# Performance work log

Hardware: AMD Instinct MI355X
Metric: run time of the kernel (lower is better)

## Reference

```python
import jax, jax.numpy as jnp
import numpy as np

N_EMBD = 2048
N_HEAD = 16
N_INNER = 8192
EPS = 1e-5


def _wn_weight(v, g):
    # torch weight_norm with dim=1 on weight [out, in]:
    # w[:, j] = g[j] * v[:, j] / ||v[:, j]||_2
    norm = jnp.sqrt(jnp.sum(v * v, axis=0))  # [in]
    return v * (g / norm)[None, :]


def _layer_norm(x, gamma, beta):
    mu = jnp.mean(x, axis=-1, keepdims=True)
    var = jnp.mean(jnp.square(x - mu), axis=-1, keepdims=True)
    return (x - mu) * jax.lax.rsqrt(var + EPS) * gamma + beta


def setup_inputs() -> dict:
    key = jax.random.key(0)
    ks = jax.random.split(key, 12)
    E, I, H = N_EMBD, N_INNER, N_HEAD
    s = lambda n: 1.0 / np.sqrt(n)
    return {
        "hidden_states": jax.random.normal(ks[0], (2, 2048, E), jnp.float32),
        "ln1_g": jnp.ones((E,), jnp.float32),
        "ln1_b": jnp.zeros((E,), jnp.float32),
        "w_qkv": jax.random.normal(ks[1], (3 * E, E), jnp.float32) * s(E),
        "b_qkv": jnp.zeros((3 * E,), jnp.float32),
        "attn_proj_v": jax.random.normal(ks[2], (E, E), jnp.float32) * s(E),
        "attn_proj_g": jnp.abs(jax.random.normal(ks[3], (E,), jnp.float32)) + 0.5,
        "attn_proj_b": jnp.zeros((E,), jnp.float32),
        "emotion_bias": jax.random.normal(ks[4], (H,), jnp.float32) * 0.1,
        "ln2_g": jnp.ones((E,), jnp.float32),
        "ln2_b": jnp.zeros((E,), jnp.float32),
        "w_fc": jax.random.normal(ks[5], (I, E), jnp.float32) * s(E),
        "b_fc": jnp.zeros((I,), jnp.float32),
        "mlp_proj_v": jax.random.normal(ks[6], (E, I), jnp.float32) * s(I),
        "mlp_proj_g": jnp.abs(jax.random.normal(ks[7], (I,), jnp.float32)) + 0.5,
        "mlp_proj_b": jnp.zeros((E,), jnp.float32),
    }


def reference(hidden_states, ln1_g, ln1_b, w_qkv, b_qkv, attn_proj_v, attn_proj_g,
              attn_proj_b, emotion_bias, ln2_g, ln2_b, w_fc, b_fc,
              mlp_proj_v, mlp_proj_g, mlp_proj_b):
    B, S, E = hidden_states.shape
    H = N_HEAD
    D = E // H

    # --- attention sub-block ---
    residual = hidden_states
    x = _layer_norm(hidden_states, ln1_g, ln1_b)
    qkv = x @ w_qkv.T + b_qkv                       # [B,S,3E]
    q, k, v = jnp.split(qkv, 3, axis=-1)
    q = q.reshape(B, S, H, D).transpose(0, 2, 1, 3)  # [B,H,S,D]
    k = k.reshape(B, S, H, D).transpose(0, 2, 1, 3)
    v = v.reshape(B, S, H, D).transpose(0, 2, 1, 3)

    scores = jnp.einsum("bhqd,bhkd->bhqk", q, k) / jnp.sqrt(jnp.float32(D))
    scores = scores + emotion_bias[None, :, None, None]
    probs = jax.nn.softmax(scores, axis=-1)
    attn = jnp.einsum("bhqk,bhkd->bhqd", probs, v)   # [B,H,S,D]
    attn = attn.transpose(0, 2, 1, 3).reshape(B, S, E)
    w_proj = _wn_weight(attn_proj_v, attn_proj_g)
    attn = attn @ w_proj.T + attn_proj_b

    hidden = attn + residual

    # --- MLP sub-block ---
    residual = hidden
    x = _layer_norm(hidden, ln2_g, ln2_b)
    h = jax.nn.gelu(x @ w_fc.T + b_fc, approximate=False)
    w_proj2 = _wn_weight(mlp_proj_v, mlp_proj_g)
    h = h @ w_proj2.T + mlp_proj_b
    return residual + h
```

## Files before the change

kernel.cpp:

```cpp
#include <hip/hip_runtime.h>
#include <hip/hip_bf16.h>

#define DEVI __device__ __forceinline__

typedef __attribute__((ext_vector_type(8))) __bf16 bf16x8;
typedef __attribute__((ext_vector_type(4))) float f32x4;
typedef __attribute__((ext_vector_type(4))) unsigned short u16x4;
typedef __attribute__((ext_vector_type(8))) unsigned short u16x8;

DEVI unsigned short f2bf(float f) {
  unsigned int u = __float_as_uint(f);
  u += 0x7FFFu + ((u >> 16) & 1u);
  return (unsigned short)(u >> 16);
}
DEVI float bf2f(unsigned short u) {
  return __uint_as_float(((unsigned int)u) << 16);
}

#define GLD16(g, l) __builtin_amdgcn_global_load_lds(                      \
    (const __attribute__((address_space(1))) void*)(g),                    \
    (__attribute__((address_space(3))) void*)(l), 16, 0, 0)


__global__ __launch_bounds__(256) void cast_k(const float* __restrict__ in,
                                              unsigned short* __restrict__ out,
                                              int n4) {
  for (int i = blockIdx.x * 256 + threadIdx.x; i < n4; i += gridDim.x * 256) {
    f32x4 v = ((const f32x4*)in)[i];
    u16x4 o;
    o.x = f2bf(v.x); o.y = f2bf(v.y); o.z = f2bf(v.z); o.w = f2bf(v.w);
    ((u16x4*)out)[i] = o;
  }
}

__global__ __launch_bounds__(256) void colnorm1_k(const float* __restrict__ v,
                                                  float* __restrict__ part,
                                                  int cols) {
  const int tid = threadIdx.x;
  const int g = tid & 127;
  const int s = tid >> 7;
  const int c0 = blockIdx.x * 512;
  const int r0 = blockIdx.y * 64 + s * 32;
  const float* base = v + (size_t)r0 * cols + c0 + g * 4;
  f32x4 acc = {};
#pragma unroll 4
  for (int i = 0; i < 32; ++i) {
    f32x4 x = *(const f32x4*)(base + (size_t)i * cols);
    acc.x += x.x * x.x; acc.y += x.y * x.y;
    acc.z += x.z * x.z; acc.w += x.w * x.w;
  }
  __shared__ f32x4 red[256];
  red[tid] = acc;
  __syncthreads();
  if (s == 0) {
    f32x4 a = red[tid], b = red[tid + 128];
    f32x4 o;
    o.x = a.x + b.x; o.y = a.y + b.y; o.z = a.z + b.z; o.w = a.w + b.w;
    *(f32x4*)(part + (size_t)blockIdx.y * cols + c0 + g * 4) = o;
  }
}

__global__ __launch_bounds__(256) void colnorm2_k(const float* __restrict__ part,
                                                  const float* __restrict__ g,
                                                  float* __restrict__ s,
                                                  int cols, int nrc) {
  const int c = blockIdx.x * 256 + threadIdx.x;
  float acc = 0.f;
  for (int i = 0; i < nrc; ++i) acc += part[(size_t)i * cols + c];
  s[c] = g[c] * rsqrtf(acc);
}

__global__ __launch_bounds__(256) void scale_cast_k(const float* __restrict__ in,
                                                    const float* __restrict__ s,
                                                    unsigned short* __restrict__ out,
                                                    int cols, int n4) {
  const int cmask4 = (cols >> 2) - 1;
  for (int i = blockIdx.x * 256 + threadIdx.x; i < n4; i += gridDim.x * 256) {
    f32x4 v = ((const f32x4*)in)[i];
    f32x4 sv = ((const f32x4*)s)[i & cmask4];
    u16x4 o;
    o.x = f2bf(v.x * sv.x); o.y = f2bf(v.y * sv.y);
    o.z = f2bf(v.z * sv.z); o.w = f2bf(v.w * sv.w);
    ((u16x4*)out)[i] = o;
  }
}

__global__ __launch_bounds__(256) void ln_k(const float* __restrict__ x,
                                            const float* __restrict__ g,
                                            const float* __restrict__ b,
                                            unsigned short* __restrict__ out) {
  const int tid = threadIdx.x, lane = tid & 63, wid = tid >> 6;
  const int row = blockIdx.x;
  const float* xr = x + (size_t)row * 2048;
  f32x4 a0 = ((const f32x4*)xr)[tid];
  f32x4 a1 = ((const f32x4*)xr)[tid + 256];
  float s = a0.x + a0.y + a0.z + a0.w + a1.x + a1.y + a1.z + a1.w;
  float ss = a0.x * a0.x + a0.y * a0.y + a0.z * a0.z + a0.w * a0.w +
             a1.x * a1.x + a1.y * a1.y + a1.z * a1.z + a1.w * a1.w;
#pragma unroll
  for (int m = 1; m < 64; m <<= 1) {
    s += __shfl_xor(s, m);
    ss += __shfl_xor(ss, m);
  }
  __shared__ float red[8];
  if (lane == 0) { red[wid] = s; red[4 + wid] = ss; }
  __syncthreads();
  s = red[0] + red[1] + red[2] + red[3];
  ss = red[4] + red[5] + red[6] + red[7];
  const float mu = s * (1.f / 2048.f);
  const float var = ss * (1.f / 2048.f) - mu * mu;
  const float rs = rsqrtf(var + 1e-5f);
  f32x4 g0 = ((const f32x4*)g)[tid], g1 = ((const f32x4*)g)[tid + 256];
  f32x4 b0 = ((const f32x4*)b)[tid], b1 = ((const f32x4*)b)[tid + 256];
  u16x4 o0, o1;
  o0.x = f2bf((a0.x - mu) * rs * g0.x + b0.x);
  o0.y = f2bf((a0.y - mu) * rs * g0.y + b0.y);
  o0.z = f2bf((a0.z - mu) * rs * g0.z + b0.z);
  o0.w = f2bf((a0.w - mu) * rs * g0.w + b0.w);
  o1.x = f2bf((a1.x - mu) * rs * g1.x + b1.x);
  o1.y = f2bf((a1.y - mu) * rs * g1.y + b1.y);
  o1.z = f2bf((a1.z - mu) * rs * g1.z + b1.z);
  o1.w = f2bf((a1.w - mu) * rs * g1.w + b1.w);
  unsigned short* orow = out + (size_t)row * 2048;
  *(u16x4*)(orow + 4 * tid) = o0;
  *(u16x4*)(orow + 1024 + 4 * tid) = o1;
}

__global__ __launch_bounds__(256) void vtrans_k(const unsigned short* __restrict__ qkv,
                                                unsigned short* __restrict__ vt) {
  __shared__ unsigned short t[64][134];
  const int tid = threadIdx.x;
  const int bh = blockIdx.x >> 5, st = blockIdx.x & 31;
  const int b = bh >> 4, h = bh & 15;
  const unsigned short* vb = qkv + (size_t)(b * 2048 + st * 64) * 6144 + 4096 + h * 128;
#pragma unroll
  for (int i = 0; i < 4; ++i) {
    int f = tid + (i << 8);
    int row = f >> 4, c8 = f & 15;
    u16x8 x = *(const u16x8*)(vb + (size_t)row * 6144 + c8 * 8);
#pragma unroll
    for (int j = 0; j < 4; ++j) {
      unsigned int pk = ((unsigned int)x[2 * j + 1] << 16) | x[2 * j];
      *(unsigned int*)&t[row][c8 * 8 + 2 * j] = pk;
    }
  }
  __syncthreads();
  const int lane = tid & 63, wid = tid >> 6;
  unsigned short* ob = vt + ((size_t)bh << 18) + (st << 6);
#pragma unroll
  for (int j = 0; j < 32; ++j) {
    int d = (wid << 5) + j;
    ob[((size_t)d << 11) + lane] = t[lane][d];
  }
}

__global__ __launch_bounds__(256) void g4red_k(const unsigned short* __restrict__ parts,
                                               const float* __restrict__ bias,
                                               const float* __restrict__ res,
                                               float* __restrict__ out, int n4) {
  const size_t PS = (size_t)4096 * 2048;
  for (int i = blockIdx.x * 256 + threadIdx.x; i < n4; i += gridDim.x * 256) {
    u16x4 a = ((const u16x4*)(parts))[i];
    u16x4 b = ((const u16x4*)(parts + PS))[i];
    u16x4 c = ((const u16x4*)(parts + 2 * PS))[i];
    u16x4 d = ((const u16x4*)(parts + 3 * PS))[i];
    f32x4 r = ((const f32x4*)res)[i];
    f32x4 bb = ((const f32x4*)bias)[i & 511];
    f32x4 o;
    o.x = bf2f(a.x) + bf2f(b.x) + bf2f(c.x) + bf2f(d.x) + r.x + bb.x;
    o.y = bf2f(a.y) + bf2f(b.y) + bf2f(c.y) + bf2f(d.y) + r.y + bb.y;
    o.z = bf2f(a.z) + bf2f(b.z) + bf2f(c.z) + bf2f(d.z) + r.z + bb.z;
    o.w = bf2f(a.w) + bf2f(b.w) + bf2f(c.w) + bf2f(d.w) + r.w + bb.w;
    ((f32x4*)out)[i] = o;
  }
}

struct GemmP {
  const unsigned short* A;
  const unsigned short* B;
  const float* bias;
  const float* res;
  float* outF;
  unsigned short* outH;
  int M, N, K;
};

DEVI void gemm128_body(const GemmP& p, int m0, int n0, int k0, int nk) {
  const int tid = threadIdx.x, lane = tid & 63, wid = tid >> 6;
  const int K = p.K;
  const int wr = wid >> 1, wc = wid & 1;

  __shared__ __align__(16) unsigned short sA[2][4096];
  __shared__ __align__(16) unsigned short sB[2][4096];

  const int c0 = tid, c1 = tid + 256;
  const unsigned short* gA0 = p.A + (size_t)(m0 + (c0 >> 2)) * K + k0 + ((c0 & 3) << 3);
  const unsigned short* gA1 = p.A + (size_t)(m0 + (c1 >> 2)) * K + k0 + ((c1 & 3) << 3);
  const unsigned short* gB0 = p.B + (size_t)(n0 + (c0 >> 2)) * K + k0 + ((c0 & 3) << 3);
  const unsigned short* gB1 = p.B + (size_t)(n0 + (c1 >> 2)) * K + k0 + ((c1 & 3) << 3);
  const int l0 = wid << 9, l1 = (wid << 9) + 2048;

  f32x4 acc[4][4] = {};
  const int arow = (wr << 6) + (lane & 15);
  const int brow = (wc << 6) + (lane & 15);
  const int koff = (lane >> 4) << 3;

#define STAGE128(bufi, t) do { int ko = (t) << 5;       \
    GLD16(gA0 + ko, &sA[bufi][l0]);                     \
    GLD16(gA1 + ko, &sA[bufi][l1]);                     \
    GLD16(gB0 + ko, &sB[bufi][l0]);                     \
    GLD16(gB1 + ko, &sB[bufi][l1]); } while (0)

  STAGE128(0, 0);
  __syncthreads();
  int cur = 0;
  for (int t = 0; t < nk; ++t) {
    if (t + 1 < nk) STAGE128(cur ^ 1, t + 1);
    bf16x8 af[4], bfr[4];
#pragma unroll
    for (int i = 0; i < 4; ++i)
      af[i] = *(const bf16x8*)&sA[cur][(arow + (i << 4)) * 32 + koff];
#pragma unroll
    for (int i = 0; i < 4; ++i)
      bfr[i] = *(const bf16x8*)&sB[cur][(brow + (i << 4)) * 32 + koff];
#pragma unroll
    for (int i = 0; i < 4; ++i)
#pragma unroll
      for (int j = 0; j < 4; ++j)
        acc[i][j] = __builtin_amdgcn_mfma_f32_16x16x32_bf16(af[i], bfr[j], acc[i][j], 0, 0, 0);
    __syncthreads();
    cur ^= 1;
  }
#undef STAGE128

  const int rbase = m0 + (wr << 6) + ((lane >> 4) << 2);
  const int cbase = n0 + (wc << 6) + (lane & 15);
#pragma unroll
  for (int mi = 0; mi < 4; ++mi) {
#pragma unroll
    for (int ni = 0; ni < 4; ++ni) {
      const int col = cbase + (ni << 4);
#pragma unroll
      for (int r = 0; r < 4; ++r) {
        const int row = rbase + (mi << 4) + r;
        const size_t o = (size_t)row * p.N + col;
        p.outF[o] = acc[mi][ni][r] + p.bias[col] + p.res[o];
      }
    }
  }
}

__global__ __launch_bounds__(256) void g2_proj128(GemmP p) {
  const int x = blockIdx.x & 7, i = blockIdx.x >> 3;
  const int bm = (x >> 1) * 8 + (i >> 3);
  const int bn = (x & 1) * 8 + (i & 7);
  gemm128_body(p, bm << 7, bn << 7, 0, p.K >> 5);
}

DEVI void setup256(const GemmP& p, int m0, int n0, int k0,
                   const unsigned short*& gsA0, const unsigned short*& gsA1,
                   const unsigned short*& gsB0, const unsigned short*& gsB1) {
  const int tid = threadIdx.x;
  int r_[2], c_[2];
#pragma unroll
  for (int j = 0; j < 2; ++j) {
    int d = tid * 16 + j * 8192;
    int w = (d & 1023) ^ (((d >> 9) & 1) << 5);
    r_[j] = ((d >> 10) << 4) + (w >> 6);
    c_[j] = (w & 63) >> 1;
  }
  gsA0 = p.A + (size_t)(m0 + r_[0]) * p.K + k0 + c_[0];
  gsA1 = p.A + (size_t)(m0 + r_[1]) * p.K + k0 + c_[1];
  gsB0 = p.B + (size_t)(n0 + r_[0]) * p.K + k0 + c_[0];
  gsB1 = p.B + (size_t)(n0 + r_[1]) * p.K + k0 + c_[1];
}

template <int EPI>
DEVI void epi256(const GemmP& p, f32x4 (&acc)[8][4], int m0, int n0,
                 unsigned short* outH) {
  const int lane = threadIdx.x & 63, wid = threadIdx.x >> 6;
  const int wr = wid >> 2, wc = wid & 3;
  const int lr = lane & 15, lk = lane >> 4;
  const int rbase = m0 + wr * 128 + (lk << 2);
  const int cbase = n0 + wc * 64 + lr;
#pragma unroll
  for (int m = 0; m < 8; ++m) {
#pragma unroll
    for (int n = 0; n < 4; ++n) {
      const int col = cbase + (n << 4);
      const float bb = (EPI == 5) ? 0.f : p.bias[col];
#pragma unroll
      for (int r = 0; r < 4; ++r) {
        const int row = rbase + (m << 4) + r;
        float v = acc[m][n][r] + bb;
        if constexpr (EPI == 2) {
          float y = 0.7978845608028654f * (v + 0.044715f * v * v * v);
          float u = __expf(2.f * y);
          v = (y > 40.f) ? v : v * (u / (u + 1.f));
        }
        outH[(size_t)row * p.N + col] = f2bf(v);
      }
    }
  }
}

template <int EPI>
DEVI void gemm2p_body(const GemmP& p, unsigned short* lds_raw, int m0, int n0,
                      int k0, int nk, unsigned short* outH) {
  const int tid = threadIdx.x, lane = tid & 63, wid = tid >> 6;
  const int wr = wid >> 2, wc = wid & 3;
  const int lr = lane & 15, lk = lane >> 4;
  const int fb = (lr * 64 + lk * 16) ^ ((lr & 8) << 2);

  const unsigned short *gsA0, *gsA1, *gsB0, *gsB1;
  setup256(p, m0, n0, k0, gsA0, gsA1, gsB0, gsB1);

#define STG2(b, kt) do { unsigned short* _d = lds_raw + ((b) << 14);     \
    GLD16(gsA0 + ((size_t)(kt) << 5), _d + (tid << 3));                  \
    GLD16(gsA1 + ((size_t)(kt) << 5), _d + 4096 + (tid << 3));           \
    GLD16(gsB0 + ((size_t)(kt) << 5), _d + 8192 + (tid << 3));           \
    GLD16(gsB1 + ((size_t)(kt) << 5), _d + 12288 + (tid << 3)); } while (0)

  f32x4 acc[8][4] = {};
  STG2(0, 0);
  __syncthreads();
  int cur = 0;
  for (int t = 0; t < nk; ++t) {
    if (t + 1 < nk) STG2(cur ^ 1, t + 1);
    const char* tA = (const char*)(lds_raw + (cur << 14));
    const char* tB = tA + 16384;
    bf16x8 a_[8], b_[4];
#pragma unroll
    for (int n = 0; n < 4; ++n)
      b_[n] = *(const bf16x8*)(tB + (((wc << 2) + n) << 10) + fb);
#pragma unroll
    for (int m = 0; m < 8; ++m)
      a_[m] = *(const bf16x8*)(tA + (((wr << 3) + m) << 10) + fb);
#pragma unroll
    for (int m = 0; m < 8; ++m)
#pragma unroll
      for (int n = 0; n < 4; ++n)
        acc[m][n] = __builtin_amdgcn_mfma_f32_16x16x32_bf16(a_[m], b_[n], acc[m][n], 0, 0, 0);
    __syncthreads();
    cur ^= 1;
  }
#undef STG2
  epi256<EPI>(p, acc, m0, n0, outH);
}

template <int EPI>
DEVI void gemmr2k64_body(const GemmP& p, unsigned short* lds_raw, int m0, int n0,
                         int k0, int nk64, unsigned short* outH) {
  const int tid = threadIdx.x, lane = tid & 63, wid = tid >> 6;
  const int wr = wid >> 2, wc = wid & 3;
  const int lr = lane & 15, lk = lane >> 4;
  const int fb = (lr * 64 + lk * 16) ^ ((lr & 8) << 2);

  const unsigned short *gsA0, *gsA1, *gsB0, *gsB1;
  setup256(p, m0, n0, k0, gsA0, gsA1, gsB0, gsB1);

#define STG64(bufi, kt) do { unsigned short* _d = lds_raw + ((bufi) << 15);  \
    int _ko = (kt) << 6;                                                     \
    GLD16(gsA0 + _ko,      _d + (tid << 3));                                 \
    GLD16(gsA1 + _ko,      _d + 4096 + (tid << 3));                          \
    GLD16(gsA0 + _ko + 32, _d + 8192 + (tid << 3));                          \
    GLD16(gsA1 + _ko + 32, _d + 12288 + (tid << 3));                         \
    GLD16(gsB0 + _ko,      _d + 16384 + (tid << 3));                         \
    GLD16(gsB1 + _ko,      _d + 20480 + (tid << 3));                         \
    GLD16(gsB0 + _ko + 32, _d + 24576 + (tid << 3));                         \
    GLD16(gsB1 + _ko + 32, _d + 28672 + (tid << 3)); } while (0)

  f32x4 acc[8][4] = {};
  STG64(0, 0);
  asm volatile("s_waitcnt vmcnt(0)" ::: "memory");
  __builtin_amdgcn_s_barrier();
  asm volatile("" ::: "memory");

  for (int t = 0; t < nk64; ++t) {
    if (t + 1 < nk64) STG64((t + 1) & 1, t + 1);
    const char* base = (const char*)(lds_raw + ((t & 1) << 15));
#pragma unroll
    for (int s = 0; s < 2; ++s) {
      const char* tA = base + s * 16384;
      const char* tB = base + 32768 + s * 16384;
      bf16x8 a_[8], b_[4];
#pragma unroll
      for (int n = 0; n < 4; ++n)
        b_[n] = *(const bf16x8*)(tB + (((wc << 2) + n) << 10) + fb);
#pragma unroll
      for (int m = 0; m < 8; ++m)
        a_[m] = *(const bf16x8*)(tA + (((wr << 3) + m) << 10) + fb);
      __builtin_amdgcn_s_setprio(1);
#pragma unroll
      for (int m = 0; m < 8; ++m)
#pragma unroll
        for (int n = 0; n < 4; ++n)
          acc[m][n] = __builtin_amdgcn_mfma_f32_16x16x32_bf16(a_[m], b_[n], acc[m][n], 0, 0, 0);
      __builtin_amdgcn_s_setprio(0);
    }
    if (t + 1 < nk64) asm volatile("s_waitcnt vmcnt(0)" ::: "memory");
    __builtin_amdgcn_s_barrier();
    asm volatile("" ::: "memory");
  }
#undef STG64
  epi256<EPI>(p, acc, m0, n0, outH);
}

__global__ __launch_bounds__(512, 2) void g1_qkv256(GemmP p) {
  extern __shared__ unsigned short lds_raw[];
  const int x = blockIdx.x & 7, i = blockIdx.x >> 3;
  const int bm = (x & 1) * 8 + (i & 7);
  const int bn = (x >> 1) * 6 + (i >> 3);
  gemm2p_body<0>(p, lds_raw, bm << 8, bn << 8, 0, p.K >> 5, p.outH);
}
__global__ __launch_bounds__(512, 1) void g3_fc64(GemmP p) {
  extern __shared__ unsigned short lds_raw[];
  const int x = blockIdx.x & 7, i = blockIdx.x >> 3;
  const int bm = (x & 1) * 8 + (i & 7);
  const int bn = (x >> 1) * 8 + (i >> 3);
  gemmr2k64_body<2>(p, lds_raw, bm << 8, bn << 8, 0, 32, p.outH);
}
__global__ __launch_bounds__(512, 1) void g4_sk64(GemmP p) {
  extern __shared__ unsigned short lds_raw[];
  const int x = blockIdx.x & 7, i = blockIdx.x >> 3;
  const int ks = x & 3;
  const int bm = (x >> 2) * 8 + (i >> 3);
  const int bn = i & 7;
  unsigned short* outH = p.outH + (size_t)ks * 4096 * 2048;
  gemmr2k64_body<5>(p, lds_raw, bm << 8, bn << 8, ks << 11, 32, outH);
}

__global__ __launch_bounds__(512) void attn_k(const unsigned short* __restrict__ qkv,
                                              const unsigned short* __restrict__ Vt,
                                              unsigned short* __restrict__ O) {
  const int tid = threadIdx.x, lane = tid & 63, wid = tid >> 6;
  const int bid = blockIdx.x;
  const int pos = bid >> 3;
  const int bh = (bid & 7) * 4 + (pos >> 4);
  const int qt = pos & 15;
  const int q0 = qt * 128 + wid * 16;
  const int b = bh >> 4, h = bh & 15;
  const float C = 0.08838834764831845f * 1.4426950408889634f;

  __shared__ __align__(16) unsigned short sK[64 * 128];
  __shared__ __align__(16) unsigned short sV[128 * 64];
  __shared__ __align__(16) unsigned short sP[8][16 * 72];

  const unsigned short* Qb = qkv + (size_t)(b * 2048) * 6144 + h * 128;
  const unsigned short* Kb = qkv + (size_t)(b * 2048) * 6144 + 2048 + h * 128;
  const unsigned short* Vb = Vt + ((size_t)bh << 18);

  bf16x8 qf[4];
  {
    const unsigned short* qp = Qb + (size_t)(q0 + (lane & 15)) * 6144 + ((lane >> 4) << 3);
#pragma unroll
    for (int kk = 0; kk < 4; ++kk) qf[kk] = *(const bf16x8*)(qp + kk * 32);
  }

  int koffs[2], voffs[2];
#pragma unroll
  for (int i = 0; i < 2; ++i) {
    const int c = tid + (i << 9);
    const int kv = c >> 4, jj = c & 15;
    const int js = (jj & 8) | ((jj ^ kv) & 7);
    koffs[i] = kv * 6144 + (js << 3);
    const int d = c >> 3, j2 = c & 7;
    const int js2 = j2 ^ (d & 7);
    voffs[i] = d * 2048 + (js2 << 3);
  }
  u16x8 kreg[2], vreg[2];
  auto PREF = [&](int kt) {
    const int kv0 = kt << 6;
    const unsigned short* kb = Kb + (size_t)kv0 * 6144;
#pragma unroll
    for (int i = 0; i < 2; ++i) {
      kreg[i] = *(const u16x8*)(kb + koffs[i]);
      vreg[i] = *(const u16x8*)(Vb + kv0 + voffs[i]);
    }
  };

  f32x4 oacc[8] = {};
  float mrun = -3e38f, lrun = 0.f;
  PREF(0);

  for (int kt = 0; kt < 32; ++kt) {
#pragma unroll
    for (int i = 0; i < 2; ++i) {
      const int c8 = (tid + (i << 9)) << 3;
      *(u16x8*)&sK[c8] = kreg[i];
      *(u16x8*)&sV[c8] = vreg[i];
    }
    __syncthreads();
    if (kt + 1 < 32) PREF(kt + 1);

    f32x4 sc[4] = {};
    __builtin_amdgcn_s_setprio(1);
#pragma unroll
    for (int ti = 0; ti < 4; ++ti) {
#pragma unroll
      for (int kk = 0; kk < 4; ++kk) {
        const int row = (ti << 4) + (lane & 15);
        int bo = (row << 8) + (kk << 6) + ((lane >> 4) << 4);
        bo ^= (row & 7) << 4;
        bf16x8 kf = *(const bf16x8*)((const char*)sK + bo);
        sc[ti] = __builtin_amdgcn_mfma_f32_16x16x32_bf16(kf, qf[kk], sc[ti], 0, 0, 0);
      }
    }
    __builtin_amdgcn_s_setprio(0);

    float pv[16];
    float mx = -3e38f;
#pragma unroll
    for (int ti = 0; ti < 4; ++ti)
#pragma unroll
      for (int r = 0; r < 4; ++r) {
        float x = sc[ti][r];
        pv[(ti << 2) + r] = x;
        mx = fmaxf(mx, x);
      }
    mx = fmaxf(mx, __shfl_xor(mx, 16));
    mx = fmaxf(mx, __shfl_xor(mx, 32));

    float corr = 1.f;
    if (!__all(mx - mrun <= 90.50966799f)) {
      const float mnew = fmaxf(mrun, mx);
      corr = exp2f((mrun - mnew) * C);
      mrun = mnew;
      float fr[4];
#pragma unroll
      for (int r = 0; r < 4; ++r) fr[r] = __shfl(corr, ((lane >> 4) << 2) + r);
#pragma unroll
      for (int di = 0; di < 8; ++di)
#pragma unroll
        for (int r = 0; r < 4; ++r) oacc[di][r] *= fr[r];
    }
    float psum = 0.f;
#pragma unroll
    for (int i2 = 0; i2 < 16; ++i2) {
      float e = exp2f((pv[i2] - mrun) * C);
      pv[i2] = e;
      psum += e;
    }
    psum += __shfl_xor(psum, 16);
    psum += __shfl_xor(psum, 32);
    lrun = lrun * corr + psum;

    unsigned short* prow = &sP[wid][(lane & 15) * 72];
#pragma unroll
    for (int ti = 0; ti < 4; ++ti) {
      u16x4 w4;
      w4.x = f2bf(pv[(ti << 2) + 0]);
      w4.y = f2bf(pv[(ti << 2) + 1]);
      w4.z = f2bf(pv[(ti << 2) + 2]);
      w4.w = f2bf(pv[(ti << 2) + 3]);
      *(u16x4*)&prow[(ti << 4) + ((lane >> 4) << 2)] = w4;
    }

    bf16x8 pfA, pfB;
    {
      const char* pb = (const char*)&sP[wid][0] + (lane & 15) * 144 + ((lane >> 4) << 4);
      pfA = *(const bf16x8*)(pb);
      pfB = *(const bf16x8*)(pb + 64);
    }
    __builtin_amdgcn_s_setprio(1);
#pragma unroll
    for (int di = 0; di < 8; ++di) {
#pragma unroll
      for (int ks = 0; ks < 2; ++ks) {
        const int dr = (di << 4) + (lane & 15);
        int bo = (dr << 7) + (ks << 6) + ((lane >> 4) << 4);
        bo ^= (dr & 7) << 4;
        bf16x8 vf = *(const bf16x8*)((const char*)sV + bo);
        oacc[di] = __builtin_amdgcn_mfma_f32_16x16x32_bf16(ks ? pfB : pfA, vf, oacc[di], 0, 0, 0);
      }
    }
    __builtin_amdgcn_s_setprio(0);
    __syncthreads();
  }

  float il[4];
#pragma unroll
  for (int r = 0; r < 4; ++r) il[r] = 1.f / __shfl(lrun, ((lane >> 4) << 2) + r);
  const size_t obase = ((size_t)(b * 2048 + q0)) * 2048 + h * 128;
#pragma unroll
  for (int di = 0; di < 8; ++di)
#pragma unroll
    for (int r = 0; r < 4; ++r) {
      const size_t o = obase + (size_t)(((lane >> 4) << 2) + r) * 2048 + (di << 4) + (lane & 15);
      O[o] = f2bf(oacc[di][r] * il[r]);
    }
}


extern "C" void kernel_launch(void* const* d_in, const int* in_sizes, int n_in,
                              void* d_out, int out_size, void* d_ws, size_t ws_size,
                              hipStream_t stream) {
  (void)in_sizes; (void)n_in; (void)out_size; (void)ws_size;
  const float* hidden = (const float*)d_in[0];
  const float* ln1_g = (const float*)d_in[1];
  const float* ln1_b = (const float*)d_in[2];
  const float* w_qkv = (const float*)d_in[3];
  const float* b_qkv = (const float*)d_in[4];
  const float* apv = (const float*)d_in[5];
  const float* apg = (const float*)d_in[6];
  const float* apb = (const float*)d_in[7];
  const float* ln2_g = (const float*)d_in[9];
  const float* ln2_b = (const float*)d_in[10];
  const float* w_fc = (const float*)d_in[11];
  const float* b_fc = (const float*)d_in[12];
  const float* mpv = (const float*)d_in[13];
  const float* mpg = (const float*)d_in[14];
  const float* mpb = (const float*)d_in[15];

  char* w = (char*)d_ws;
  const size_t MBs = 1ull << 20;
  unsigned short* xln = (unsigned short*)(w + 0);
  float* hidden2 = (float*)(w + 0);
  unsigned short* vtbuf = (unsigned short*)(w + 32 * MBs);
  unsigned short* hbuf = (unsigned short*)(w + 32 * MBs);
  unsigned short* qkv = (unsigned short*)(w + 96 * MBs);
  unsigned short* wfc_bf = (unsigned short*)(w + 96 * MBs);
  unsigned short* partH = (unsigned short*)(w + 96 * MBs);
  unsigned short* xln2 = (unsigned short*)(w + 128 * MBs);
  unsigned short* attn_out = (unsigned short*)(w + 144 * MBs);
  unsigned short* wqkv_bf = (unsigned short*)(w + 160 * MBs);
  unsigned short* w2_bf = (unsigned short*)(w + 160 * MBs);
  unsigned short* wproj_bf = (unsigned short*)(w + 192 * MBs);
  float* s_attn = (float*)(w + 200 * MBs);
  float* s_mlp = (float*)(w + 200 * MBs + 32768);
  float* part_attn = (float*)(w + 201 * MBs);
  float* part_mlp = (float*)(w + 202 * MBs);

  hipFuncSetAttribute((const void*)g1_qkv256, hipFuncAttributeMaxDynamicSharedMemorySize, 65536);
  hipFuncSetAttribute((const void*)g3_fc64, hipFuncAttributeMaxDynamicSharedMemorySize, 131072);
  hipFuncSetAttribute((const void*)g4_sk64, hipFuncAttributeMaxDynamicSharedMemorySize, 131072);

  cast_k<<<2048, 256, 0, stream>>>(w_qkv, wqkv_bf, (6144 * 2048) / 4);
  colnorm1_k<<<dim3(4, 32), 256, 0, stream>>>(apv, part_attn, 2048);
  colnorm2_k<<<8, 256, 0, stream>>>(part_attn, apg, s_attn, 2048, 32);
  scale_cast_k<<<2048, 256, 0, stream>>>(apv, s_attn, wproj_bf, 2048, (2048 * 2048) / 4);
  colnorm1_k<<<dim3(16, 32), 256, 0, stream>>>(mpv, part_mlp, 8192);
  colnorm2_k<<<32, 256, 0, stream>>>(part_mlp, mpg, s_mlp, 8192, 32);

  ln_k<<<4096, 256, 0, stream>>>(hidden, ln1_g, ln1_b, xln);

  GemmP p1 = {xln, wqkv_bf, b_qkv, nullptr, nullptr, qkv, 4096, 6144, 2048};
  g1_qkv256<<<384, 512, 65536, stream>>>(p1);

  vtrans_k<<<1024, 256, 0, stream>>>(qkv, vtbuf);

  attn_k<<<512, 512, 0, stream>>>(qkv, vtbuf, attn_out);

  cast_k<<<2048, 256, 0, stream>>>(w_fc, wfc_bf, (8192 * 2048) / 4);
  scale_cast_k<<<4096, 256, 0, stream>>>(mpv, s_mlp, w2_bf, 8192, (2048 * 8192) / 4);

  GemmP p2 = {attn_out, wproj_bf, apb, hidden, hidden2, nullptr, 4096, 2048, 2048};
  g2_proj128<<<512, 256, 0, stream>>>(p2);

  ln_k<<<4096, 256, 0, stream>>>(hidden2, ln2_g, ln2_b, xln2);

  GemmP p3 = {xln2, wfc_bf, b_fc, nullptr, nullptr, hbuf, 4096, 8192, 2048};
  g3_fc64<<<512, 512, 131072, stream>>>(p3);

  GemmP p4 = {hbuf, w2_bf, mpb, nullptr, nullptr, partH, 4096, 2048, 8192};
  g4_sk64<<<512, 512, 131072, stream>>>(p4);
  g4red_k<<<2048, 256, 0, stream>>>(partH, mpb, hidden2, (float*)d_out,
                                    (4096 * 2048) / 4);
}
```

Baseline: 735.8 us.

## Use 8-phase ping-pong pipelined GEMM body for FC layer

```diff
diff --git a/kernel.cpp b/kernel.cpp
--- a/kernel.cpp
+++ b/kernel.cpp
@@ -406,6 +406,99 @@
   epi256<EPI>(p, acc, m0, n0, outH);
 }
 
+template <int EPI>
+DEVI void gemm8p_body(const GemmP& p, unsigned short* lds_raw, int m0, int n0,
+                      int k0, int nt, unsigned short* outH) {
+  const int tid = threadIdx.x, lane = tid & 63, wid = tid >> 6;
+  const int wr = wid >> 2, wc = wid & 3;
+  const int lr = lane & 15, lk = lane >> 4;
+  const int fb = (lr * 64 + lk * 16) ^ ((lr & 8) << 2);
+  char* Lc = (char*)lds_raw;
+
+  const unsigned short *gsA0, *gsA1, *gsB0, *gsB1;
+  setup256(p, m0, n0, k0, gsA0, gsA1, gsB0, gsB1);
+
+#define STGH(bufb, h, gp, tt) do {                                        \
+    char* _d = Lc + ((bufb) << 16) + ((h) << 14) + tid * 16;              \
+    GLD16((gp) + ((size_t)(tt) << 6),      _d);                           \
+    GLD16((gp) + ((size_t)(tt) << 6) + 32, _d + 8192); } while (0)
+
+  const char* Abase = Lc + (wr << 14);
+  const char* Bbase = Lc + 32768 + ((wc >> 1) << 14);
+  const int bg = (wc & 1) << 2;
+
+#define RDA(dst, bufb, mq) do {                                           \
+    const char* _a = Abase + ((bufb) << 16);                              \
+    _Pragma("unroll") for (int mi = 0; mi < 4; ++mi)                      \
+      _Pragma("unroll") for (int ks = 0; ks < 2; ++ks)                    \
+        dst[mi][ks] = *(const bf16x8*)(_a + ks * 8192 +                   \
+                        (((mq) * 4 + mi) << 10) + fb); } while (0)
+#define RDB(bufb, nq) do {                                                \
+    const char* _b = Bbase + ((bufb) << 16);                              \
+    _Pragma("unroll") for (int ni = 0; ni < 2; ++ni)                      \
+      _Pragma("unroll") for (int ks = 0; ks < 2; ++ks)                    \
+        bq[ni][ks] = *(const bf16x8*)(_b + ks * 8192 +                    \
+                        ((bg + (nq) * 2 + ni) << 10) + fb); } while (0)
+#define MFMAQ(av, mq, nq) do {                                            \
+    __builtin_amdgcn_s_setprio(1);                                        \
+    _Pragma("unroll") for (int mi = 0; mi < 4; ++mi)                      \
+      _Pragma("unroll") for (int ni = 0; ni < 2; ++ni)                    \
+        _Pragma("unroll") for (int ks = 0; ks < 2; ++ks)                  \
+          acc[(mq) * 4 + mi][(nq) * 2 + ni] =                             \
+            __builtin_amdgcn_mfma_f32_16x16x32_bf16(                      \
+              av[mi][ks], bq[ni][ks], acc[(mq) * 4 + mi][(nq) * 2 + ni],  \
+              0, 0, 0);                                                   \
+    __builtin_amdgcn_s_setprio(0); } while (0)
+#define BAR __builtin_amdgcn_s_barrier()
+#define LGKM0 do { asm volatile("s_waitcnt lgkmcnt(0)" ::: "memory");     \
+                   __builtin_amdgcn_sched_barrier(0); } while (0)
+
+  f32x4 acc[8][4] = {};
+  bf16x8 aq[4][2], a2[4][2], bq[2][2];
+
+  STGH(0, 0, gsA0, 0); STGH(0, 1, gsA1, 0); STGH(0, 2, gsB0, 0); STGH(0, 3, gsB1, 0);
+  STGH(1, 0, gsA0, 1); STGH(1, 1, gsA1, 1); STGH(1, 2, gsB0, 1); STGH(1, 3, gsB1, 1);
+  asm volatile("s_waitcnt vmcnt(0)" ::: "memory");
+  BAR;
+  asm volatile("" ::: "memory");
+
+  const int NIT = nt >> 1;
+  for (int i = 0; i < NIT; ++i) {
+    const int T = 2 * i;
+    const bool G2 = (T + 2 < nt), G3 = (T + 3 < nt);
+    RDA(aq, 0, 0); RDB(0, 0);
+    BAR; LGKM0; MFMAQ(aq, 0, 0); BAR;
+    RDA(a2, 0, 1);
+    BAR; LGKM0; MFMAQ(a2, 1, 0); BAR;
+    RDB(0, 1);
+    if (G2) STGH(0, 0, gsA0, T + 2);
+    BAR; LGKM0; MFMAQ(aq, 0, 1); BAR;
+    if (G2) STGH(0, 1, gsA1, T + 2);
+    asm volatile("s_waitcnt vmcnt(4)" ::: "memory");
+    BAR; MFMAQ(a2, 1, 1); BAR;
+    RDA(aq, 1, 0); RDB(1, 0);
+    if (G2) STGH(0, 2, gsB0, T + 2);
+    BAR; LGKM0; MFMAQ(aq, 0, 0); BAR;
+    RDA(a2, 1, 1);
+    if (G2) STGH(0, 3, gsB1, T + 2);
+    BAR; LGKM0; MFMAQ(a2, 1, 0); BAR;
+    RDB(1, 1);
+    if (G3) { STGH(1, 0, gsA0, T + 3); STGH(1, 1, gsA1, T + 3); }
+    BAR; LGKM0; MFMAQ(aq, 0, 1); BAR;
+    if (G3) { STGH(1, 2, gsB0, T + 3); STGH(1, 3, gsB1, T + 3); }
+    asm volatile("s_waitcnt vmcnt(8)" ::: "memory");
+    BAR; MFMAQ(a2, 1, 1); BAR;
+    asm volatile("" ::: "memory");
+  }
+#undef STGH
+#undef RDA
+#undef RDB
+#undef MFMAQ
+#undef BAR
+#undef LGKM0
+  epi256<EPI>(p, acc, m0, n0, outH);
+}
+
 __global__ __launch_bounds__(512, 2) void g1_qkv256(GemmP p) {
   extern __shared__ unsigned short lds_raw[];
   const int x = blockIdx.x & 7, i = blockIdx.x >> 3;
@@ -413,12 +506,12 @@
   const int bn = (x >> 1) * 6 + (i >> 3);
   gemm2p_body<0>(p, lds_raw, bm << 8, bn << 8, 0, p.K >> 5, p.outH);
 }
-__global__ __launch_bounds__(512, 1) void g3_fc64(GemmP p) {
+__global__ __launch_bounds__(512, 1) void g3_fc8p(GemmP p) {
   extern __shared__ unsigned short lds_raw[];
   const int x = blockIdx.x & 7, i = blockIdx.x >> 3;
   const int bm = (x & 1) * 8 + (i & 7);
   const int bn = (x >> 1) * 8 + (i >> 3);
-  gemmr2k64_body<2>(p, lds_raw, bm << 8, bn << 8, 0, 32, p.outH);
+  gemm8p_body<2>(p, lds_raw, bm << 8, bn << 8, 0, 32, p.outH);
 }
 __global__ __launch_bounds__(512, 1) void g4_sk64(GemmP p) {
   extern __shared__ unsigned short lds_raw[];
@@ -632,7 +725,7 @@
   float* part_mlp = (float*)(w + 202 * MBs);
 
   hipFuncSetAttribute((const void*)g1_qkv256, hipFuncAttributeMaxDynamicSharedMemorySize, 65536);
-  hipFuncSetAttribute((const void*)g3_fc64, hipFuncAttributeMaxDynamicSharedMemorySize, 131072);
+  hipFuncSetAttribute((const void*)g3_fc8p, hipFuncAttributeMaxDynamicSharedMemorySize, 131072);
   hipFuncSetAttribute((const void*)g4_sk64, hipFuncAttributeMaxDynamicSharedMemorySize, 131072);
 
   cast_k<<<2048, 256, 0, stream>>>(w_qkv, wqkv_bf, (6144 * 2048) / 4);
@@ -660,7 +753,7 @@
   ln_k<<<4096, 256, 0, stream>>>(hidden2, ln2_g, ln2_b, xln2);
 
   GemmP p3 = {xln2, wfc_bf, b_fc, nullptr, nullptr, hbuf, 4096, 8192, 2048};
-  g3_fc64<<<512, 512, 131072, stream>>>(p3);
+  g3_fc8p<<<512, 512, 131072, stream>>>(p3);
 
   GemmP p4 = {hbuf, w2_bf, mpb, nullptr, nullptr, partH, 4096, 2048, 8192};
   g4_sk64<<<512, 512, 131072, stream>>>(p4);
```

After: 733.3 us. About the same (-0.3%).

## Split attention KV into two halves with combine pass; merge small prep kernels

Applied to the files above, without the earlier changes.

```diff
diff --git a/kernel.cpp b/kernel.cpp
--- a/kernel.cpp
+++ b/kernel.cpp
@@ -22,10 +22,9 @@
     (__attribute__((address_space(3))) void*)(l), 16, 0, 0)
 
 
-__global__ __launch_bounds__(256) void cast_k(const float* __restrict__ in,
-                                              unsigned short* __restrict__ out,
-                                              int n4) {
-  for (int i = blockIdx.x * 256 + threadIdx.x; i < n4; i += gridDim.x * 256) {
+DEVI void cast_body(int blk, int nblk, const float* __restrict__ in,
+                    unsigned short* __restrict__ out, int n4) {
+  for (int i = blk * 256 + threadIdx.x; i < n4; i += nblk * 256) {
     f32x4 v = ((const f32x4*)in)[i];
     u16x4 o;
     o.x = f2bf(v.x); o.y = f2bf(v.y); o.z = f2bf(v.z); o.w = f2bf(v.w);
@@ -33,14 +32,27 @@
   }
 }
 
-__global__ __launch_bounds__(256) void colnorm1_k(const float* __restrict__ v,
-                                                  float* __restrict__ part,
-                                                  int cols) {
+DEVI void scale_cast_body(int blk, int nblk, const float* __restrict__ in,
+                          const float* __restrict__ s,
+                          unsigned short* __restrict__ out, int cols, int n4) {
+  const int cmask4 = (cols >> 2) - 1;
+  for (int i = blk * 256 + threadIdx.x; i < n4; i += nblk * 256) {
+    f32x4 v = ((const f32x4*)in)[i];
+    f32x4 sv = ((const f32x4*)s)[i & cmask4];
+    u16x4 o;
+    o.x = f2bf(v.x * sv.x); o.y = f2bf(v.y * sv.y);
+    o.z = f2bf(v.z * sv.z); o.w = f2bf(v.w * sv.w);
+    ((u16x4*)out)[i] = o;
+  }
+}
+
+DEVI void colnorm1_body(int bx, int by, const float* __restrict__ v,
+                        float* __restrict__ part, int cols) {
   const int tid = threadIdx.x;
   const int g = tid & 127;
   const int s = tid >> 7;
-  const int c0 = blockIdx.x * 512;
-  const int r0 = blockIdx.y * 64 + s * 32;
+  const int c0 = bx * 512;
+  const int r0 = by * 64 + s * 32;
   const float* base = v + (size_t)r0 * cols + c0 + g * 4;
   f32x4 acc = {};
 #pragma unroll 4
@@ -49,48 +61,29 @@
     acc.x += x.x * x.x; acc.y += x.y * x.y;
     acc.z += x.z * x.z; acc.w += x.w * x.w;
   }
-  __shared__ f32x4 red[256];
-  red[tid] = acc;
+  __shared__ f32x4 red1[256];
+  red1[tid] = acc;
   __syncthreads();
   if (s == 0) {
-    f32x4 a = red[tid], b = red[tid + 128];
+    f32x4 a = red1[tid], b = red1[tid + 128];
     f32x4 o;
     o.x = a.x + b.x; o.y = a.y + b.y; o.z = a.z + b.z; o.w = a.w + b.w;
-    *(f32x4*)(part + (size_t)blockIdx.y * cols + c0 + g * 4) = o;
-  }
-}
-
-__global__ __launch_bounds__(256) void colnorm2_k(const float* __restrict__ part,
-                                                  const float* __restrict__ g,
-                                                  float* __restrict__ s,
-                                                  int cols, int nrc) {
-  const int c = blockIdx.x * 256 + threadIdx.x;
+    *(f32x4*)(part + (size_t)by * cols + c0 + g * 4) = o;
+  }
+}
+
+DEVI void colnorm2_body(int blk, const float* __restrict__ part,
+                        const float* __restrict__ g, float* __restrict__ s,
+                        int cols, int nrc) {
+  const int c = blk * 256 + threadIdx.x;
   float acc = 0.f;
   for (int i = 0; i < nrc; ++i) acc += part[(size_t)i * cols + c];
   s[c] = g[c] * rsqrtf(acc);
 }
 
-__global__ __launch_bounds__(256) void scale_cast_k(const float* __restrict__ in,
-                                                    const float* __restrict__ s,
-                                                    unsigned short* __restrict__ out,
-                                                    int cols, int n4) {
-  const int cmask4 = (cols >> 2) - 1;
-  for (int i = blockIdx.x * 256 + threadIdx.x; i < n4; i += gridDim.x * 256) {
-    f32x4 v = ((const f32x4*)in)[i];
-    f32x4 sv = ((const f32x4*)s)[i & cmask4];
-    u16x4 o;
-    o.x = f2bf(v.x * sv.x); o.y = f2bf(v.y * sv.y);
-    o.z = f2bf(v.z * sv.z); o.w = f2bf(v.w * sv.w);
-    ((u16x4*)out)[i] = o;
-  }
-}
-
-__global__ __launch_bounds__(256) void ln_k(const float* __restrict__ x,
-                                            const float* __restrict__ g,
-                                            const float* __restrict__ b,
-                                            unsigned short* __restrict__ out) {
+DEVI void ln_body(int row, const float* __restrict__ x, const float* __restrict__ g,
+                  const float* __restrict__ b, unsigned short* __restrict__ out) {
   const int tid = threadIdx.x, lane = tid & 63, wid = tid >> 6;
-  const int row = blockIdx.x;
   const float* xr = x + (size_t)row * 2048;
   f32x4 a0 = ((const f32x4*)xr)[tid];
   f32x4 a1 = ((const f32x4*)xr)[tid + 256];
@@ -102,11 +95,11 @@
     s += __shfl_xor(s, m);
     ss += __shfl_xor(ss, m);
   }
-  __shared__ float red[8];
-  if (lane == 0) { red[wid] = s; red[4 + wid] = ss; }
+  __shared__ float red2[8];
+  if (lane == 0) { red2[wid] = s; red2[4 + wid] = ss; }
   __syncthreads();
-  s = red[0] + red[1] + red[2] + red[3];
-  ss = red[4] + red[5] + red[6] + red[7];
+  s = red2[0] + red2[1] + red2[2] + red2[3];
+  ss = red2[4] + red2[5] + red2[6] + red2[7];
   const float mu = s * (1.f / 2048.f);
   const float var = ss * (1.f / 2048.f) - mu * mu;
   const float rs = rsqrtf(var + 1e-5f);
@@ -126,11 +119,11 @@
   *(u16x4*)(orow + 1024 + 4 * tid) = o1;
 }
 
-__global__ __launch_bounds__(256) void vtrans_k(const unsigned short* __restrict__ qkv,
-                                                unsigned short* __restrict__ vt) {
-  __shared__ unsigned short t[64][134];
+DEVI void vtrans_body(int bid, const unsigned short* __restrict__ qkv,
+                      unsigned short* __restrict__ vt) {
+  __shared__ unsigned short tsh[64][134];
   const int tid = threadIdx.x;
-  const int bh = blockIdx.x >> 5, st = blockIdx.x & 31;
+  const int bh = bid >> 5, st = bid & 31;
   const int b = bh >> 4, h = bh & 15;
   const unsigned short* vb = qkv + (size_t)(b * 2048 + st * 64) * 6144 + 4096 + h * 128;
 #pragma unroll
@@ -141,7 +134,7 @@
 #pragma unroll
     for (int j = 0; j < 4; ++j) {
       unsigned int pk = ((unsigned int)x[2 * j + 1] << 16) | x[2 * j];
-      *(unsigned int*)&t[row][c8 * 8 + 2 * j] = pk;
+      *(unsigned int*)&tsh[row][c8 * 8 + 2 * j] = pk;
     }
   }
   __syncthreads();
@@ -150,8 +143,90 @@
 #pragma unroll
   for (int j = 0; j < 32; ++j) {
     int d = (wid << 5) + j;
-    ob[((size_t)d << 11) + lane] = t[lane][d];
-  }
+    ob[((size_t)d << 11) + lane] = tsh[lane][d];
+  }
+}
+
+DEVI void combine_body(int blk, const unsigned short* __restrict__ po,
+                       const float* __restrict__ marr, const float* __restrict__ larr,
+                       unsigned short* __restrict__ O) {
+  const size_t PS = (size_t)32 * 2048 * 128;
+  const float C = 0.08838834764831845f * 1.4426950408889634f;
+  const int tid = threadIdx.x;
+  const int row = blk * 32 + (tid >> 3);
+  const int bh = row >> 11, q = row & 2047;
+  const int d0 = (tid & 7) * 16;
+  const float m0 = marr[row], m1 = marr[65536 + row];
+  const float l0 = larr[row], l1 = larr[65536 + row];
+  const float M = fmaxf(m0, m1);
+  const float w0 = exp2f((m0 - M) * C), w1 = exp2f((m1 - M) * C);
+  const float inv = 1.f / (l0 * w0 + l1 * w1);
+  const float s0 = w0 * inv, s1 = w1 * inv;
+  const unsigned short* p0 = po + ((size_t)row << 7) + d0;
+  const unsigned short* p1 = p0 + PS;
+  const int b = bh >> 4, h = bh & 15;
+  unsigned short* ob = O + ((size_t)(b * 2048 + q)) * 2048 + h * 128 + d0;
+#pragma unroll
+  for (int c = 0; c < 2; ++c) {
+    u16x8 a = *(const u16x8*)(p0 + c * 8);
+    u16x8 bb = *(const u16x8*)(p1 + c * 8);
+    u16x8 o;
+#pragma unroll
+    for (int j = 0; j < 8; ++j)
+      o[j] = f2bf(bf2f(a[j]) * s0 + bf2f(bb[j]) * s1);
+    *(u16x8*)(ob + c * 8) = o;
+  }
+}
+
+
+__global__ __launch_bounds__(256) void prep1_k(const float* wq, unsigned short* wqb,
+                                               const float* apv, float* part_a,
+                                               const float* mpv, float* part_m,
+                                               const float* hid, const float* g1v,
+                                               const float* b1v, unsigned short* xln) {
+  const int blk = blockIdx.x;
+  if (blk < 2048)       cast_body(blk, 2048, wq, wqb, (6144 * 2048) / 4);
+  else if (blk < 2176) { int i = blk - 2048; colnorm1_body(i & 3, i >> 2, apv, part_a, 2048); }
+  else if (blk < 2688) { int i = blk - 2176; colnorm1_body(i & 15, i >> 4, mpv, part_m, 8192); }
+  else                  ln_body(blk - 2688, hid, g1v, b1v, xln);
+}
+
+__global__ __launch_bounds__(256) void prep2_k(const float* part_a, const float* apg,
+                                               float* s_attn, const float* part_m,
+                                               const float* mpg, float* s_mlp) {
+  const int blk = blockIdx.x;
+  if (blk < 8) colnorm2_body(blk, part_a, apg, s_attn, 2048, 32);
+  else         colnorm2_body(blk - 8, part_m, mpg, s_mlp, 8192, 32);
+}
+
+__global__ __launch_bounds__(256) void mid_k(const unsigned short* qkv,
+                                             unsigned short* vt,
+                                             const float* apv, const float* s_attn,
+                                             unsigned short* wproj_bf) {
+  const int blk = blockIdx.x;
+  if (blk < 1024) vtrans_body(blk, qkv, vt);
+  else            scale_cast_body(blk - 1024, 2048, apv, s_attn, wproj_bf, 2048,
+                                  (2048 * 2048) / 4);
+}
+
+__global__ __launch_bounds__(256) void post_k(const unsigned short* po,
+                                              const float* marr, const float* larr,
+                                              unsigned short* attn_out,
+                                              const float* wfc, unsigned short* wfc_bf,
+                                              const float* mpv, const float* s_mlp,
+                                              unsigned short* w2_bf) {
+  const int blk = blockIdx.x;
+  if (blk < 2048)       combine_body(blk, po, marr, larr, attn_out);
+  else if (blk < 4096)  cast_body(blk - 2048, 2048, wfc, wfc_bf, (8192 * 2048) / 4);
+  else                  scale_cast_body(blk - 4096, 2048, mpv, s_mlp, w2_bf, 8192,
+                                        (2048 * 8192) / 4);
+}
+
+__global__ __launch_bounds__(256) void ln_k(const float* __restrict__ x,
+                                            const float* __restrict__ g,
+                                            const float* __restrict__ b,
+                                            unsigned short* __restrict__ out) {
+  ln_body(blockIdx.x, x, g, b, out);
 }
 
 __global__ __launch_bounds__(256) void g4red_k(const unsigned short* __restrict__ parts,
@@ -432,14 +507,18 @@
 
 __global__ __launch_bounds__(512) void attn_k(const unsigned short* __restrict__ qkv,
                                               const unsigned short* __restrict__ Vt,
-                                              unsigned short* __restrict__ O) {
+                                              unsigned short* __restrict__ po,
+                                              float* __restrict__ marr,
+                                              float* __restrict__ larr) {
   const int tid = threadIdx.x, lane = tid & 63, wid = tid >> 6;
   const int bid = blockIdx.x;
-  const int pos = bid >> 3;
-  const int bh = (bid & 7) * 4 + (pos >> 4);
-  const int qt = pos & 15;
+  const int j = bid >> 3;
+  const int bh = (bid & 7) * 4 + (j >> 5);
+  const int rest = j & 31;
+  const int qt = rest >> 1, kvh = rest & 1;
   const int q0 = qt * 128 + wid * 16;
   const int b = bh >> 4, h = bh & 15;
+  const int kt0 = kvh << 4;
   const float C = 0.08838834764831845f * 1.4426950408889634f;
 
   __shared__ __align__(16) unsigned short sK[64 * 128];
@@ -481,9 +560,9 @@
 
   f32x4 oacc[8] = {};
   float mrun = -3e38f, lrun = 0.f;
-  PREF(0);
-
-  for (int kt = 0; kt < 32; ++kt) {
+  PREF(kt0);
+
+  for (int kt = 0; kt < 16; ++kt) {
 #pragma unroll
     for (int i = 0; i < 2; ++i) {
       const int c8 = (tid + (i << 9)) << 3;
@@ -491,7 +570,7 @@
       *(u16x8*)&sV[c8] = vreg[i];
     }
     __syncthreads();
-    if (kt + 1 < 32) PREF(kt + 1);
+    if (kt + 1 < 16) PREF(kt0 + kt + 1);
 
     f32x4 sc[4] = {};
     __builtin_amdgcn_s_setprio(1);
@@ -578,17 +657,20 @@
     __syncthreads();
   }
 
-  float il[4];
-#pragma unroll
-  for (int r = 0; r < 4; ++r) il[r] = 1.f / __shfl(lrun, ((lane >> 4) << 2) + r);
-  const size_t obase = ((size_t)(b * 2048 + q0)) * 2048 + h * 128;
+  const size_t PS = (size_t)32 * 2048 * 128;
+  unsigned short* pob = po + (size_t)kvh * PS + ((size_t)bh << 18);
 #pragma unroll
   for (int di = 0; di < 8; ++di)
 #pragma unroll
     for (int r = 0; r < 4; ++r) {
-      const size_t o = obase + (size_t)(((lane >> 4) << 2) + r) * 2048 + (di << 4) + (lane & 15);
-      O[o] = f2bf(oacc[di][r] * il[r]);
-    }
+      const size_t o = (size_t)(q0 + ((lane >> 4) << 2) + r) * 128 + (di << 4) + (lane & 15);
+      pob[o] = f2bf(oacc[di][r]);
+    }
+  if (lane < 16) {
+    const int idx = kvh * 65536 + (bh << 11) + q0 + lane;
+    marr[idx] = mrun;
+    larr[idx] = lrun;
+  }
 }
 
 
@@ -615,6 +697,7 @@
   char* w = (char*)d_ws;
   const size_t MBs = 1ull << 20;
   unsigned short* xln = (unsigned short*)(w + 0);
+  unsigned short* po = (unsigned short*)(w + 0);
   float* hidden2 = (float*)(w + 0);
   unsigned short* vtbuf = (unsigned short*)(w + 32 * MBs);
   unsigned short* hbuf = (unsigned short*)(w + 32 * MBs);
@@ -630,29 +713,26 @@
   float* s_mlp = (float*)(w + 200 * MBs + 32768);
   float* part_attn = (float*)(w + 201 * MBs);
   float* part_mlp = (float*)(w + 202 * MBs);
+  float* marr = (float*)(w + 203 * MBs);
+  float* larr = (float*)(w + 203 * MBs + (1 << 19));
 
   hipFuncSetAttribute((const void*)g1_qkv256, hipFuncAttributeMaxDynamicSharedMemorySize, 65536);
   hipFuncSetAttribute((const void*)g3_fc64, hipFuncAttributeMaxDynamicSharedMemorySize, 131072);
   hipFuncSetAttribute((const void*)g4_sk64, hipFuncAttributeMaxDynamicSharedMemorySize, 131072);
 
-  cast_k<<<2048, 256, 0, stream>>>(w_qkv, wqkv_bf, (6144 * 2048) / 4);
-  colnorm1_k<<<dim3(4, 32), 256, 0, stream>>>(apv, part_attn, 2048);
-  colnorm2_k<<<8, 256, 0, stream>>>(part_attn, apg, s_attn, 2048, 32);
-  scale_cast_k<<<2048, 256, 0, stream>>>(apv, s_attn, wproj_bf, 2048, (2048 * 2048) / 4);
-  colnorm1_k<<<dim3(16, 32), 256, 0, stream>>>(mpv, part_mlp, 8192);
-  colnorm2_k<<<32, 256, 0, stream>>>(part_mlp, mpg, s_mlp, 8192, 32);
-
-  ln_k<<<4096, 256, 0, stream>>>(hidden, ln1_g, ln1_b, xln);
+  prep1_k<<<6784, 256, 0, stream>>>(w_qkv, wqkv_bf, apv, part_attn, mpv, part_mlp,
+                                    hidden, ln1_g, ln1_b, xln);
+  prep2_k<<<40, 256, 0, stream>>>(part_attn, apg, s_attn, part_mlp, mpg, s_mlp);
 
   GemmP p1 = {xln, wqkv_bf, b_qkv, nullptr, nullptr, qkv, 4096, 6144, 2048};
   g1_qkv256<<<384, 512, 65536, stream>>>(p1);
 
-  vtrans_k<<<1024, 256, 0, stream>>>(qkv, vtbuf);
-
-  attn_k<<<512, 512, 0, stream>>>(qkv, vtbuf, attn_out);
-
-  cast_k<<<2048, 256, 0, stream>>>(w_fc, wfc_bf, (8192 * 2048) / 4);
-  scale_cast_k<<<4096, 256, 0, stream>>>(mpv, s_mlp, w2_bf, 8192, (2048 * 8192) / 4);
+  mid_k<<<3072, 256, 0, stream>>>(qkv, vtbuf, apv, s_attn, wproj_bf);
+
+  attn_k<<<1024, 512, 0, stream>>>(qkv, vtbuf, po, marr, larr);
+
+  post_k<<<6144, 256, 0, stream>>>(po, marr, larr, attn_out, w_fc, wfc_bf,
+                                   mpv, s_mlp, w2_bf);
 
   GemmP p2 = {attn_out, wproj_bf, apb, hidden, hidden2, nullptr, 4096, 2048, 2048};
   g2_proj128<<<512, 256, 0, stream>>>(p2);
```

After: 728.0 us. About the same (-1.1%).
